# Optimization experiments

Hardware: AMD Instinct MI355X
Metric: run time of the kernel (lower is better)

The kernel has to match this reference:

```python
import jax, jax.numpy as jnp
import numpy as np

N = 100000
E = 3200000
IN_DIM = 128
HD = 64
HEADS = 4
NEG_SLOPE = 0.2


def setup_inputs() -> dict:
    key = jax.random.key(0)
    ks = jax.random.split(key, 12)
    s = lambda fan_in: 1.0 / np.sqrt(fan_in)
    x = jax.random.normal(ks[0], (N, IN_DIM), dtype=jnp.float32)
    edge_index = jax.random.randint(ks[1], (2, E), 0, N, dtype=jnp.int64)
    W1 = jax.random.normal(ks[2], (IN_DIM, HEADS * HD), dtype=jnp.float32) * s(IN_DIM)
    a_src1 = jax.random.normal(ks[3], (HEADS, HD), dtype=jnp.float32) * s(HD)
    a_dst1 = jax.random.normal(ks[4], (HEADS, HD), dtype=jnp.float32) * s(HD)
    b1 = jnp.zeros((HEADS * HD,), dtype=jnp.float32)
    W2 = jax.random.normal(ks[5], (HEADS * HD, HD), dtype=jnp.float32) * s(HEADS * HD)
    a_src2 = jax.random.normal(ks[6], (1, HD), dtype=jnp.float32) * s(HD)
    a_dst2 = jax.random.normal(ks[7], (1, HD), dtype=jnp.float32) * s(HD)
    b2 = jnp.zeros((HD,), dtype=jnp.float32)
    lin_w = jax.random.normal(ks[8], (HD, 2), dtype=jnp.float32) * s(HD)
    lin_b = jnp.zeros((2,), dtype=jnp.float32)
    return {"x": x, "edge_index": edge_index, "W1": W1, "a_src1": a_src1,
            "a_dst1": a_dst1, "b1": b1, "W2": W2, "a_src2": a_src2,
            "a_dst2": a_dst2, "b2": b2, "lin_w": lin_w, "lin_b": lin_b}


def gat_conv(x, src, dst, W, a_src, a_dst, bias, heads, out_dim, concat):
    n = x.shape[0]
    h = (x @ W).reshape(n, heads, out_dim)                 # [N,H,D]
    alpha_s = jnp.einsum('nhd,hd->nh', h, a_src)           # [N,H]
    alpha_d = jnp.einsum('nhd,hd->nh', h, a_dst)           # [N,H]
    e = alpha_s[src] + alpha_d[dst]                        # [Etot,H]
    e = jnp.where(e > 0, e, NEG_SLOPE * e)                 # leaky relu
    m = jax.ops.segment_max(e, dst, num_segments=n)        # scatter-softmax (stable)
    m = jnp.where(jnp.isfinite(m), m, 0.0)
    e = jnp.exp(e - m[dst])
    denom = jax.ops.segment_sum(e, dst, num_segments=n)
    alpha = e / denom[dst]                                 # [Etot,H]
    out = jax.ops.segment_sum(h[src] * alpha[:, :, None], dst, num_segments=n)  # [N,H,D]
    out = out.reshape(n, heads * out_dim) if concat else out.mean(axis=1)
    return out + bias


def reference(x, edge_index, W1, a_src1, a_dst1, b1, W2, a_src2, a_dst2, b2, lin_w, lin_b):
    n = x.shape[0]
    loops = jnp.arange(n, dtype=edge_index.dtype)
    src = jnp.concatenate([edge_index[0], loops])          # add self-loops (PyG default)
    dst = jnp.concatenate([edge_index[1], loops])
    h = gat_conv(x, src, dst, W1, a_src1, a_dst1, b1, HEADS, HD, True)
    h = jax.nn.elu(h)
    h = gat_conv(h, src, dst, W2, a_src2, a_dst2, b2, 1, HD, True)
    h = jax.nn.elu(h)
    return h @ lin_w + lin_b                               # [N,2]
```

## Files before the change

kernel.cpp:

```cpp
#include <hip/hip_runtime.h>
#include <hip/hip_fp16.h>
#include <math.h>

#define NN 100000
#define EE 3200000
#define ETOT (EE + NN)
#define NEG_SLOPE 0.2f
#define DMAX 96
#define CHUNK 4096
#define NB0 ((ETOT + CHUNK - 1) / CHUNK)
#define RB 391
#define CAP 16384

typedef _Float16 half8 __attribute__((ext_vector_type(8)));
typedef _Float16 half4v __attribute__((ext_vector_type(4)));
typedef float floatx4 __attribute__((ext_vector_type(4)));

__device__ __forceinline__ float wsum64(float v) {
#pragma unroll
  for (int o = 32; o; o >>= 1) v += __shfl_xor(v, o);
  return v;
}
__device__ __forceinline__ float lrelu(float v) { return v > 0.f ? v : NEG_SLOPE * v; }
__device__ __forceinline__ float elu1(float v) { return v > 0.f ? v : expm1f(v); }

__global__ void k_init(int* __restrict__ ccur) {
  ccur[threadIdx.x] = threadIdx.x * CAP;
}

__global__ __launch_bounds__(256) void k_pass1(const int* __restrict__ ei,
                                               int* __restrict__ ccur,
                                               unsigned* __restrict__ ebuf,
                                               const float* __restrict__ W1,
                                               const float* __restrict__ W2,
                                               _Float16* __restrict__ W1t,
                                               _Float16* __restrict__ W2t) {
  int b = blockIdx.x;
  if (b >= NB0) {
    int idx = (b - NB0) * 256 + threadIdx.x;
    if (idx < 32768) {
      int n = idx >> 7, k = idx & 127;
      W1t[idx] = (_Float16)W1[k * 256 + n];
    } else {
      int j = idx - 32768;
      int n = j >> 8, k = j & 255;
      W2t[j] = (_Float16)W2[k * 64 + n];
    }
    return;
  }
  __shared__ unsigned vv[CHUNK];
  __shared__ unsigned short cbv[CHUNK];
  __shared__ int h[256];
  __shared__ int cur[256];
  int t = threadIdx.x;
  h[t] = 0;
  __syncthreads();
  int base = b * CHUNK;
  int lim = base + CHUNK; if (lim > ETOT) lim = ETOT;
  int cnt = lim - base;
  for (int i = t; i < cnt; i += 256) {
    int e = base + i;
    int s, d;
    if (e < EE) { s = ei[e]; d = ei[EE + e]; } else { s = e - EE; d = s; }
    unsigned cb = (unsigned)d / (unsigned)RB;
    unsigned dloc = (unsigned)d - cb * (unsigned)RB;
    vv[i] = (dloc << 17) | (unsigned)s;
    cbv[i] = (unsigned short)cb;
    atomicAdd(&h[cb], 1);
  }
  __syncthreads();
  if (h[t]) cur[t] = atomicAdd(&ccur[t], h[t]);
  __syncthreads();
  for (int i = t; i < cnt; i += 256) {
    int cb = cbv[i];
    int pos = atomicAdd(&cur[cb], 1);
    ebuf[pos] = vv[i];
  }
}

__global__ __launch_bounds__(256) void k_pass2(const unsigned* __restrict__ ebuf,
                                               const int* __restrict__ ccur,
                                               int* __restrict__ offs,
                                               int* __restrict__ degarr,
                                               int* __restrict__ csr) {
  __shared__ unsigned ed[CAP];
  __shared__ int hist[RB];
  __shared__ int cur[RB];
  int b = blockIdx.x, t = threadIdx.x;
  int d0 = b * RB;
  int rb = NN - d0; if (rb > RB) rb = RB;
  int w0 = b * CAP;
  int cnt = ccur[b] - w0;
  if (cnt > CAP) cnt = CAP;
  for (int j = t; j < rb; j += 256) hist[j] = 0;
  __syncthreads();
  for (int i = t; i < cnt; i += 256) {
    unsigned v = ebuf[w0 + i];
    ed[i] = v;
    atomicAdd(&hist[v >> 17], 1);
  }
  __syncthreads();
  if (t == 0) {
    int run = w0;
    for (int j = 0; j < rb; ++j) { cur[j] = run; run += hist[j]; }
  }
  __syncthreads();
  for (int j = t; j < rb; j += 256) {
    offs[d0 + j] = cur[j];
    degarr[d0 + j] = hist[j];
  }
  __syncthreads();
  for (int i = t; i < cnt; i += 256) {
    unsigned v = ed[i];
    int pos = atomicAdd(&cur[v >> 17], 1);
    csr[pos] = (int)(v & 0x1FFFFu);
  }
}

__global__ __launch_bounds__(256) void k_gemm1m(const float* __restrict__ x,
                                                const _Float16* __restrict__ W1t,
                                                const float* __restrict__ a_src,
                                                const float* __restrict__ a_dst,
                                                _Float16* __restrict__ h1h,
                                                float* __restrict__ as_out,
                                                float* __restrict__ ad_out) {
  __shared__ _Float16 As[64][136];
  __shared__ _Float16 Wt[128][136];
  const int bx = blockIdx.x & 1;
  const int by = blockIdx.x >> 1;
  const int tid = threadIdx.x;
  const int row0 = by * 64;
#pragma unroll
  for (int i = 0; i < 8; ++i) {
    int idx = i * 256 + tid;
    int r = idx >> 5;
    int c4 = (idx & 31) * 4;
    int gr = row0 + r;
    float4 f = make_float4(0.f, 0.f, 0.f, 0.f);
    if (gr < NN) f = *(const float4*)(x + (size_t)gr * 128 + c4);
    half4v h; h[0] = (_Float16)f.x; h[1] = (_Float16)f.y; h[2] = (_Float16)f.z; h[3] = (_Float16)f.w;
    *(half4v*)&As[r][c4] = h;
  }
#pragma unroll
  for (int i = 0; i < 8; ++i) {
    int idx = i * 256 + tid;
    int r = idx >> 4;
    int g = idx & 15;
    *(half8*)&Wt[r][g * 8] = *(const half8*)(W1t + (size_t)(bx * 128 + r) * 128 + g * 8);
  }
  __syncthreads();

  const int wid = tid >> 6, lane = tid & 63;
  const int m16 = lane & 15, quad = lane >> 4;
  floatx4 acc[8];
#pragma unroll
  for (int nt = 0; nt < 8; ++nt) acc[nt] = (floatx4){0.f, 0.f, 0.f, 0.f};
#pragma unroll
  for (int ks = 0; ks < 4; ++ks) {
    half8 av = *(half8*)&As[wid * 16 + m16][ks * 32 + quad * 8];
#pragma unroll
    for (int nt = 0; nt < 8; ++nt) {
      half8 bv = *(half8*)&Wt[nt * 16 + m16][ks * 32 + quad * 8];
      acc[nt] = __builtin_amdgcn_mfma_f32_16x16x32_f16(av, bv, acc[nt], 0, 0, 0);
    }
  }
  float asr[8], adr[8];
#pragma unroll
  for (int nt = 0; nt < 8; ++nt) {
    asr[nt] = a_src[bx * 128 + nt * 16 + m16];
    adr[nt] = a_dst[bx * 128 + nt * 16 + m16];
  }
#pragma unroll
  for (int r = 0; r < 4; ++r) {
    int gr = row0 + wid * 16 + quad * 4 + r;
    bool ok = gr < NN;
#pragma unroll
    for (int hp = 0; hp < 2; ++hp) {
      float ps = 0.f, pd = 0.f;
#pragma unroll
      for (int j = 0; j < 4; ++j) {
        ps = fmaf(acc[hp * 4 + j][r], asr[hp * 4 + j], ps);
        pd = fmaf(acc[hp * 4 + j][r], adr[hp * 4 + j], pd);
      }
#pragma unroll
      for (int o = 1; o < 16; o <<= 1) { ps += __shfl_xor(ps, o); pd += __shfl_xor(pd, o); }
      if (ok && m16 == 0) {
        as_out[gr * 4 + bx * 2 + hp] = ps;
        ad_out[gr * 4 + bx * 2 + hp] = pd;
      }
    }
    if (ok) {
#pragma unroll
      for (int nt = 0; nt < 8; ++nt)
        h1h[(size_t)gr * 256 + bx * 128 + nt * 16 + m16] = (_Float16)acc[nt][r];
    }
  }
}

__global__ __launch_bounds__(256) void k_gemm2m(const _Float16* __restrict__ h1e,
                                                const _Float16* __restrict__ W2t,
                                                const float* __restrict__ a_src,
                                                const float* __restrict__ a_dst,
                                                _Float16* __restrict__ h2h,
                                                float* __restrict__ as_out,
                                                float* __restrict__ ad_out) {
  __shared__ _Float16 As2[64][136];
  __shared__ _Float16 Wt2[64][264];
  const int by = blockIdx.x;
  const int tid = threadIdx.x;
  const int row0 = by * 64;
#pragma unroll
  for (int i = 0; i < 8; ++i) {
    int idx = i * 256 + tid;
    int r = idx >> 5;
    int g = idx & 31;
    *(half8*)&Wt2[r][g * 8] = *(const half8*)(W2t + (size_t)r * 256 + g * 8);
  }
  const int wid = tid >> 6, lane = tid & 63;
  const int m16 = lane & 15, quad = lane >> 4;
  floatx4 acc[4];
#pragma unroll
  for (int nt = 0; nt < 4; ++nt) acc[nt] = (floatx4){0.f, 0.f, 0.f, 0.f};

  for (int kc = 0; kc < 2; ++kc) {
#pragma unroll
    for (int i = 0; i < 4; ++i) {
      int idx = i * 256 + tid;
      int r = idx >> 4;
      int g = idx & 15;
      int gr = row0 + r;
      half8 v = {0, 0, 0, 0, 0, 0, 0, 0};
      if (gr < NN) v = *(const half8*)(h1e + (size_t)gr * 256 + kc * 128 + g * 8);
      *(half8*)&As2[r][g * 8] = v;
    }
    __syncthreads();
#pragma unroll
    for (int ks = 0; ks < 4; ++ks) {
      half8 av = *(half8*)&As2[wid * 16 + m16][ks * 32 + quad * 8];
#pragma unroll
      for (int nt = 0; nt < 4; ++nt) {
        half8 bv = *(half8*)&Wt2[nt * 16 + m16][kc * 128 + ks * 32 + quad * 8];
        acc[nt] = __builtin_amdgcn_mfma_f32_16x16x32_f16(av, bv, acc[nt], 0, 0, 0);
      }
    }
    __syncthreads();
  }
  float asr[4], adr[4];
#pragma unroll
  for (int nt = 0; nt < 4; ++nt) {
    asr[nt] = a_src[nt * 16 + m16];
    adr[nt] = a_dst[nt * 16 + m16];
  }
#pragma unroll
  for (int r = 0; r < 4; ++r) {
    float ps = 0.f, pd = 0.f;
#pragma unroll
    for (int nt = 0; nt < 4; ++nt) {
      ps = fmaf(acc[nt][r], asr[nt], ps);
      pd = fmaf(acc[nt][r], adr[nt], pd);
    }
#pragma unroll
    for (int o = 1; o < 16; o <<= 1) { ps += __shfl_xor(ps, o); pd += __shfl_xor(pd, o); }
    int gr = row0 + wid * 16 + quad * 4 + r;
    if (gr < NN) {
      if (m16 == 0) { as_out[gr] = ps; ad_out[gr] = pd; }
#pragma unroll
      for (int nt = 0; nt < 4; ++nt)
        h2h[(size_t)gr * 64 + nt * 16 + m16] = (_Float16)acc[nt][r];
    }
  }
}

__global__ __launch_bounds__(256) void k_attn1(const int* __restrict__ offs,
                                               const int* __restrict__ degarr,
                                               const int* __restrict__ csr_src,
                                               const float* __restrict__ a_s,
                                               const float* __restrict__ a_d,
                                               const _Float16* __restrict__ h1h,
                                               const float* __restrict__ b1,
                                               _Float16* __restrict__ h1e) {
  __shared__ float alpha[4][DMAX][4];
  __shared__ int sidx[4][DMAX];
  const int wid = threadIdx.x >> 6;
  const int n = blockIdx.x * 4 + wid;
  const int lane = threadIdx.x & 63;
  const int beg = offs[n], deg = degarr[n];
  const float4 ad = *(const float4*)(a_d + n * 4);
  float4 sm = make_float4(0.f, 0.f, 0.f, 0.f);
  for (int d = lane; d < deg; d += 64) {
    int s = csr_src[beg + d];
    float4 as = *(const float4*)(a_s + s * 4);
    float e0 = __expf(lrelu(as.x + ad.x));
    float e1 = __expf(lrelu(as.y + ad.y));
    float e2 = __expf(lrelu(as.z + ad.z));
    float e3 = __expf(lrelu(as.w + ad.w));
    sm.x += e0; sm.y += e1; sm.z += e2; sm.w += e3;
    if (d < DMAX) {
      sidx[wid][d] = s;
      *(float4*)&alpha[wid][d][0] = make_float4(e0, e1, e2, e3);
    }
  }
  sm.x = wsum64(sm.x); sm.y = wsum64(sm.y); sm.z = wsum64(sm.z); sm.w = wsum64(sm.w);
  const float4 inv4 = make_float4(1.f / sm.x, 1.f / sm.y, 1.f / sm.z, 1.f / sm.w);
  const int dlim = deg < DMAX ? deg : DMAX;
  for (int d = lane; d < dlim; d += 64) {
    float4 a = *(float4*)&alpha[wid][d][0];
    a.x *= inv4.x; a.y *= inv4.y; a.z *= inv4.z; a.w *= inv4.w;
    *(float4*)&alpha[wid][d][0] = a;
  }
  const int h = lane >> 4;
  float4 acc = make_float4(0.f, 0.f, 0.f, 0.f);
  int d = 0;
  for (; d + 8 <= dlim; d += 8) {
    int ss[8]; float ww[8];
#pragma unroll
    for (int u = 0; u < 8; ++u) {
      ss[u] = sidx[wid][d + u];
      ww[u] = alpha[wid][d + u][h];
    }
    half4v rr[8];
#pragma unroll
    for (int u = 0; u < 8; ++u)
      rr[u] = *(const half4v*)(h1h + (size_t)ss[u] * 256 + lane * 4);
#pragma unroll
    for (int u = 0; u < 8; ++u) {
      acc.x = fmaf((float)rr[u][0], ww[u], acc.x);
      acc.y = fmaf((float)rr[u][1], ww[u], acc.y);
      acc.z = fmaf((float)rr[u][2], ww[u], acc.z);
      acc.w = fmaf((float)rr[u][3], ww[u], acc.w);
    }
  }
  for (; d < dlim; ++d) {
    int s = sidx[wid][d];
    float w = alpha[wid][d][h];
    half4v r = *(const half4v*)(h1h + (size_t)s * 256 + lane * 4);
    acc.x = fmaf((float)r[0], w, acc.x); acc.y = fmaf((float)r[1], w, acc.y);
    acc.z = fmaf((float)r[2], w, acc.z); acc.w = fmaf((float)r[3], w, acc.w);
  }
  const float adh = (h & 2) ? ((h & 1) ? ad.w : ad.z) : ((h & 1) ? ad.y : ad.x);
  const float invh = (h & 2) ? ((h & 1) ? inv4.w : inv4.z) : ((h & 1) ? inv4.y : inv4.x);
  for (; d < deg; ++d) {
    int s = csr_src[beg + d];
    float w = __expf(lrelu(a_s[s * 4 + h] + adh)) * invh;
    half4v r = *(const half4v*)(h1h + (size_t)s * 256 + lane * 4);
    acc.x = fmaf((float)r[0], w, acc.x); acc.y = fmaf((float)r[1], w, acc.y);
    acc.z = fmaf((float)r[2], w, acc.z); acc.w = fmaf((float)r[3], w, acc.w);
  }
  const int c = lane * 4;
  float4 bb = *(const float4*)(b1 + c);
  half4v o;
  o[0] = (_Float16)elu1(acc.x + bb.x);
  o[1] = (_Float16)elu1(acc.y + bb.y);
  o[2] = (_Float16)elu1(acc.z + bb.z);
  o[3] = (_Float16)elu1(acc.w + bb.w);
  *(half4v*)(h1e + (size_t)n * 256 + c) = o;
}

__global__ __launch_bounds__(256) void k_attn2(const int* __restrict__ offs,
                                               const int* __restrict__ degarr,
                                               const int* __restrict__ csr_src,
                                               const float* __restrict__ a_s,
                                               const float* __restrict__ a_d,
                                               const _Float16* __restrict__ h2h,
                                               const float* __restrict__ b2,
                                               const float* __restrict__ lin_w,
                                               const float* __restrict__ lin_b,
                                               float* __restrict__ out) {
  __shared__ float alpha2[4][DMAX];
  __shared__ int sidx2[4][DMAX];
  const int wid = threadIdx.x >> 6;
  const int n = blockIdx.x * 4 + wid;
  const int lane = threadIdx.x & 63;
  const int beg = offs[n], deg = degarr[n];
  const float adn = a_d[n];
  float sm = 0.f;
  for (int d = lane; d < deg; d += 64) {
    int s = csr_src[beg + d];
    float e = __expf(lrelu(a_s[s] + adn));
    sm += e;
    if (d < DMAX) { sidx2[wid][d] = s; alpha2[wid][d] = e; }
  }
  sm = wsum64(sm);
  const float inv = 1.f / sm;
  const int dlim = deg < DMAX ? deg : DMAX;
  for (int d = lane; d < dlim; d += 64) alpha2[wid][d] *= inv;
  float acc = 0.f;
  int d = 0;
  for (; d + 8 <= dlim; d += 8) {
    int ss[8]; float ww[8]; float vv[8];
#pragma unroll
    for (int u = 0; u < 8; ++u) {
      ss[u] = sidx2[wid][d + u];
      ww[u] = alpha2[wid][d + u];
    }
#pragma unroll
    for (int u = 0; u < 8; ++u)
      vv[u] = (float)h2h[(size_t)ss[u] * 64 + lane];
#pragma unroll
    for (int u = 0; u < 8; ++u) acc = fmaf(vv[u], ww[u], acc);
  }
  for (; d < dlim; ++d) {
    acc = fmaf((float)h2h[(size_t)sidx2[wid][d] * 64 + lane], alpha2[wid][d], acc);
  }
  for (; d < deg; ++d) {
    int s = csr_src[beg + d];
    float w = __expf(lrelu(a_s[s] + adn)) * inv;
    acc = fmaf((float)h2h[(size_t)s * 64 + lane], w, acc);
  }
  float o = elu1(acc + b2[lane]);
  float p0 = wsum64(o * lin_w[lane * 2 + 0]);
  float p1 = wsum64(o * lin_w[lane * 2 + 1]);
  if (lane == 0) {
    out[n * 2 + 0] = p0 + lin_b[0];
    out[n * 2 + 1] = p1 + lin_b[1];
  }
}

extern "C" void kernel_launch(void* const* d_in, const int* in_sizes, int n_in,
                              void* d_out, int out_size, void* d_ws, size_t ws_size,
                              hipStream_t stream) {
  const float* x      = (const float*)d_in[0];
  const int*   ei     = (const int*)d_in[1];
  const float* W1     = (const float*)d_in[2];
  const float* a_src1 = (const float*)d_in[3];
  const float* a_dst1 = (const float*)d_in[4];
  const float* b1     = (const float*)d_in[5];
  const float* W2     = (const float*)d_in[6];
  const float* a_src2 = (const float*)d_in[7];
  const float* a_dst2 = (const float*)d_in[8];
  const float* b2     = (const float*)d_in[9];
  const float* lin_w  = (const float*)d_in[10];
  const float* lin_b  = (const float*)d_in[11];
  float* outp = (float*)d_out;

  char* w = (char*)d_ws;
  _Float16* h1h = (_Float16*)(w + 0);
  _Float16* h1e = (_Float16*)(w + 51200000);
  _Float16* h2h = (_Float16*)(w + 102400000);
  _Float16* W1t = (_Float16*)(w + 115200000);
  _Float16* W2t = (_Float16*)(w + 115265536);
  float*  as1 = (float*)(w + 115298304);
  float*  ad1 = (float*)(w + 116898304);
  float*  as2 = (float*)(w + 118498304);
  float*  ad2 = (float*)(w + 118898304);
  int*    offs = (int*)(w + 119298304);
  int*    degarr = (int*)(w + 119698304);
  int*    ccur = (int*)(w + 120098304);
  unsigned* ebuf = (unsigned*)(w + 120099328);
  int*    csr = (int*)(w + 136876544);

  k_init<<<1, 256, 0, stream>>>(ccur);
  k_pass1<<<NB0 + 192, 256, 0, stream>>>(ei, ccur, ebuf, W1, W2, W1t, W2t);
  k_pass2<<<256, 256, 0, stream>>>(ebuf, ccur, offs, degarr, csr);

  k_gemm1m<<<2 * 1563, 256, 0, stream>>>(x, W1t, a_src1, a_dst1, h1h, as1, ad1);
  k_attn1<<<NN / 4, 256, 0, stream>>>(offs, degarr, csr, as1, ad1, h1h, b1, h1e);

  k_gemm2m<<<1563, 256, 0, stream>>>(h1e, W2t, a_src2, a_dst2, h2h, as2, ad2);
  k_attn2<<<NN / 4, 256, 0, stream>>>(offs, degarr, csr, as2, ad2, h2h, b2, lin_w, lin_b, outp);
}
```

Baseline: 578.4 us.

## Split wave across multiple edges per iteration with wider vector gathers in attention

In both attention aggregation kernels the wavefront now processes several neighbor edges at once: layer 1 splits the wave into two halves that each gather 16-byte half8 rows for alternate edges, and layer 2 splits it into four groups gathering half4 chunks of the 64-wide row. Partial sums are combined with cross-lane shuffles before bias, ELU and the final linear. The aim is wider per-lane memory requests and more gathers in flight per wave, to hide latency in the random-row gather. The cost is extra shuffle reductions, more tail-handling branches, and overflow edges beyond DMAX being processed by only part of the wave.

New measurement: 574.3 us. No clear change (-0.7%).

```diff
diff --git a/kernel.cpp b/kernel.cpp
--- a/kernel.cpp
+++ b/kernel.cpp
@@ -308,52 +308,78 @@
     a.x *= inv4.x; a.y *= inv4.y; a.z *= inv4.z; a.w *= inv4.w;
     *(float4*)&alpha[wid][d][0] = a;
   }
-  const int h = lane >> 4;
-  float4 acc = make_float4(0.f, 0.f, 0.f, 0.f);
+  const int half = lane >> 5;
+  const int sub = lane & 31;
+  const int head = sub >> 3;
+  const _Float16* __restrict__ hb = h1h + sub * 8;
+  float accv[8];
+#pragma unroll
+  for (int j = 0; j < 8; ++j) accv[j] = 0.f;
   int d = 0;
   for (; d + 8 <= dlim; d += 8) {
-    int ss[8]; float ww[8];
-#pragma unroll
-    for (int u = 0; u < 8; ++u) {
-      ss[u] = sidx[wid][d + u];
-      ww[u] = alpha[wid][d + u][h];
-    }
-    half4v rr[8];
-#pragma unroll
-    for (int u = 0; u < 8; ++u)
-      rr[u] = *(const half4v*)(h1h + (size_t)ss[u] * 256 + lane * 4);
-#pragma unroll
-    for (int u = 0; u < 8; ++u) {
-      acc.x = fmaf((float)rr[u][0], ww[u], acc.x);
-      acc.y = fmaf((float)rr[u][1], ww[u], acc.y);
-      acc.z = fmaf((float)rr[u][2], ww[u], acc.z);
-      acc.w = fmaf((float)rr[u][3], ww[u], acc.w);
-    }
-  }
-  for (; d < dlim; ++d) {
+    int ss[4]; float ww[4];
+#pragma unroll
+    for (int u = 0; u < 4; ++u) {
+      int idx = d + 2 * u + half;
+      ss[u] = sidx[wid][idx];
+      ww[u] = alpha[wid][idx][head];
+    }
+    half8 rr[4];
+#pragma unroll
+    for (int u = 0; u < 4; ++u)
+      rr[u] = *(const half8*)(hb + (size_t)ss[u] * 256);
+#pragma unroll
+    for (int u = 0; u < 4; ++u) {
+#pragma unroll
+      for (int j = 0; j < 8; ++j)
+        accv[j] = fmaf((float)rr[u][j], ww[u], accv[j]);
+    }
+  }
+  for (; d + 2 <= dlim; d += 2) {
+    int idx = d + half;
+    int s = sidx[wid][idx];
+    float w = alpha[wid][idx][head];
+    half8 r = *(const half8*)(hb + (size_t)s * 256);
+#pragma unroll
+    for (int j = 0; j < 8; ++j) accv[j] = fmaf((float)r[j], w, accv[j]);
+  }
+  if (d < dlim) {
     int s = sidx[wid][d];
-    float w = alpha[wid][d][h];
-    half4v r = *(const half4v*)(h1h + (size_t)s * 256 + lane * 4);
-    acc.x = fmaf((float)r[0], w, acc.x); acc.y = fmaf((float)r[1], w, acc.y);
-    acc.z = fmaf((float)r[2], w, acc.z); acc.w = fmaf((float)r[3], w, acc.w);
-  }
-  const float adh = (h & 2) ? ((h & 1) ? ad.w : ad.z) : ((h & 1) ? ad.y : ad.x);
-  const float invh = (h & 2) ? ((h & 1) ? inv4.w : inv4.z) : ((h & 1) ? inv4.y : inv4.x);
-  for (; d < deg; ++d) {
-    int s = csr_src[beg + d];
-    float w = __expf(lrelu(a_s[s * 4 + h] + adh)) * invh;
-    half4v r = *(const half4v*)(h1h + (size_t)s * 256 + lane * 4);
-    acc.x = fmaf((float)r[0], w, acc.x); acc.y = fmaf((float)r[1], w, acc.y);
-    acc.z = fmaf((float)r[2], w, acc.z); acc.w = fmaf((float)r[3], w, acc.w);
-  }
-  const int c = lane * 4;
-  float4 bb = *(const float4*)(b1 + c);
-  half4v o;
-  o[0] = (_Float16)elu1(acc.x + bb.x);
-  o[1] = (_Float16)elu1(acc.y + bb.y);
-  o[2] = (_Float16)elu1(acc.z + bb.z);
-  o[3] = (_Float16)elu1(acc.w + bb.w);
-  *(half4v*)(h1e + (size_t)n * 256 + c) = o;
+    float w = half ? 0.f : alpha[wid][d][head];
+    half8 r = *(const half8*)(hb + (size_t)s * 256);
+#pragma unroll
+    for (int j = 0; j < 8; ++j) accv[j] = fmaf((float)r[j], w, accv[j]);
+  }
+  if (deg > DMAX) {
+    const float adh = head == 0 ? ad.x : head == 1 ? ad.y : head == 2 ? ad.z : ad.w;
+    const float invh = head == 0 ? inv4.x : head == 1 ? inv4.y : head == 2 ? inv4.z : inv4.w;
+    if (!half) {
+      for (int dd = DMAX; dd < deg; ++dd) {
+        int s = csr_src[beg + dd];
+        float w = __expf(lrelu(a_s[s * 4 + head] + adh)) * invh;
+        half8 r = *(const half8*)(hb + (size_t)s * 256);
+#pragma unroll
+        for (int j = 0; j < 8; ++j) accv[j] = fmaf((float)r[j], w, accv[j]);
+      }
+    }
+  }
+#pragma unroll
+  for (int j = 0; j < 8; ++j) accv[j] += __shfl_xor(accv[j], 32);
+  if (!half) {
+    const int c = sub * 8;
+    float4 b0 = *(const float4*)(b1 + c);
+    float4 b1v = *(const float4*)(b1 + c + 4);
+    half8 o;
+    o[0] = (_Float16)elu1(accv[0] + b0.x);
+    o[1] = (_Float16)elu1(accv[1] + b0.y);
+    o[2] = (_Float16)elu1(accv[2] + b0.z);
+    o[3] = (_Float16)elu1(accv[3] + b0.w);
+    o[4] = (_Float16)elu1(accv[4] + b1v.x);
+    o[5] = (_Float16)elu1(accv[5] + b1v.y);
+    o[6] = (_Float16)elu1(accv[6] + b1v.z);
+    o[7] = (_Float16)elu1(accv[7] + b1v.w);
+    *(half8*)(h1e + (size_t)n * 256 + c) = o;
+  }
 }
 
 __global__ __launch_bounds__(256) void k_attn2(const int* __restrict__ offs,
@@ -384,32 +410,65 @@
   const float inv = 1.f / sm;
   const int dlim = deg < DMAX ? deg : DMAX;
   for (int d = lane; d < dlim; d += 64) alpha2[wid][d] *= inv;
-  float acc = 0.f;
+  const int g = lane >> 4;
+  const int sub = lane & 15;
+  const _Float16* __restrict__ hb = h2h + sub * 4;
+  float a0 = 0.f, a1 = 0.f, a2 = 0.f, a3 = 0.f;
   int d = 0;
   for (; d + 8 <= dlim; d += 8) {
-    int ss[8]; float ww[8]; float vv[8];
-#pragma unroll
-    for (int u = 0; u < 8; ++u) {
-      ss[u] = sidx2[wid][d + u];
-      ww[u] = alpha2[wid][d + u];
-    }
-#pragma unroll
-    for (int u = 0; u < 8; ++u)
-      vv[u] = (float)h2h[(size_t)ss[u] * 64 + lane];
-#pragma unroll
-    for (int u = 0; u < 8; ++u) acc = fmaf(vv[u], ww[u], acc);
-  }
-  for (; d < dlim; ++d) {
-    acc = fmaf((float)h2h[(size_t)sidx2[wid][d] * 64 + lane], alpha2[wid][d], acc);
-  }
-  for (; d < deg; ++d) {
-    int s = csr_src[beg + d];
-    float w = __expf(lrelu(a_s[s] + adn)) * inv;
-    acc = fmaf((float)h2h[(size_t)s * 64 + lane], w, acc);
-  }
-  float o = elu1(acc + b2[lane]);
-  float p0 = wsum64(o * lin_w[lane * 2 + 0]);
-  float p1 = wsum64(o * lin_w[lane * 2 + 1]);
+    int i0 = d + g, i1 = d + 4 + g;
+    int s0 = sidx2[wid][i0], s1 = sidx2[wid][i1];
+    float w0 = alpha2[wid][i0], w1 = alpha2[wid][i1];
+    half4v r0 = *(const half4v*)(hb + (size_t)s0 * 64);
+    half4v r1 = *(const half4v*)(hb + (size_t)s1 * 64);
+    a0 = fmaf((float)r0[0], w0, a0); a1 = fmaf((float)r0[1], w0, a1);
+    a2 = fmaf((float)r0[2], w0, a2); a3 = fmaf((float)r0[3], w0, a3);
+    a0 = fmaf((float)r1[0], w1, a0); a1 = fmaf((float)r1[1], w1, a1);
+    a2 = fmaf((float)r1[2], w1, a2); a3 = fmaf((float)r1[3], w1, a3);
+  }
+  if (d + 4 <= dlim) {
+    int i0 = d + g;
+    int s0 = sidx2[wid][i0];
+    float w0 = alpha2[wid][i0];
+    half4v r0 = *(const half4v*)(hb + (size_t)s0 * 64);
+    a0 = fmaf((float)r0[0], w0, a0); a1 = fmaf((float)r0[1], w0, a1);
+    a2 = fmaf((float)r0[2], w0, a2); a3 = fmaf((float)r0[3], w0, a3);
+    d += 4;
+  }
+  if (d < dlim) {
+    int idx = d + g;
+    bool v = idx < dlim;
+    int s = sidx2[wid][v ? idx : d];
+    float w = v ? alpha2[wid][idx] : 0.f;
+    half4v r = *(const half4v*)(hb + (size_t)s * 64);
+    a0 = fmaf((float)r[0], w, a0); a1 = fmaf((float)r[1], w, a1);
+    a2 = fmaf((float)r[2], w, a2); a3 = fmaf((float)r[3], w, a3);
+  }
+  if (deg > DMAX && g == 0) {
+    for (int dd = DMAX; dd < deg; ++dd) {
+      int s = csr_src[beg + dd];
+      float w = __expf(lrelu(a_s[s] + adn)) * inv;
+      half4v r = *(const half4v*)(hb + (size_t)s * 64);
+      a0 = fmaf((float)r[0], w, a0); a1 = fmaf((float)r[1], w, a1);
+      a2 = fmaf((float)r[2], w, a2); a3 = fmaf((float)r[3], w, a3);
+    }
+  }
+  a0 += __shfl_xor(a0, 16); a1 += __shfl_xor(a1, 16);
+  a2 += __shfl_xor(a2, 16); a3 += __shfl_xor(a3, 16);
+  a0 += __shfl_xor(a0, 32); a1 += __shfl_xor(a1, 32);
+  a2 += __shfl_xor(a2, 32); a3 += __shfl_xor(a3, 32);
+  const int c = sub * 4;
+  float4 bb = *(const float4*)(b2 + c);
+  float o0 = elu1(a0 + bb.x);
+  float o1 = elu1(a1 + bb.y);
+  float o2 = elu1(a2 + bb.z);
+  float o3 = elu1(a3 + bb.w);
+  float4 lw0 = *(const float4*)(lin_w + c * 2);
+  float4 lw1 = *(const float4*)(lin_w + c * 2 + 4);
+  float p0 = o0 * lw0.x + o1 * lw0.z + o2 * lw1.x + o3 * lw1.z;
+  float p1 = o0 * lw0.y + o1 * lw0.w + o2 * lw1.y + o3 * lw1.w;
+  p0 = wsum64(p0) * 0.25f;
+  p1 = wsum64(p1) * 0.25f;
   if (lane == 0) {
     out[n * 2 + 0] = p0 + lin_b[0];
     out[n * 2 + 1] = p1 + lin_b[1];
```
